# Optimization experiments

Hardware: AMD Instinct MI355X
Metric: run time of the kernel (lower is better)

The kernel has to match this reference:

```python
import jax, jax.numpy as jnp
import numpy as np

B, N, K, H, NC, NL = 512, 128, 16, 16, 6, 4  # batch, atoms, neighbors/atom, h_a, classes, EGNN layers

def _lin(key, fi, fo):
    lim = 1.0 / np.sqrt(fi)
    return jax.random.uniform(key, (fi, fo), jnp.float32, -lim, lim)

def _bias(key, fi, fo):
    lim = 1.0 / np.sqrt(fi)
    return jax.random.uniform(key, (fo,), jnp.float32, -lim, lim)

def setup_inputs():
    key = jax.random.key(0)
    kc, ke, ki, ko, kf, kl = jax.random.split(key, 6)
    coords = jax.random.normal(kc, (B, N, 3), dtype=jnp.float32)
    # fixed adjacency: node i -> (i+1 .. i+K) mod N, same for every frame
    adj = np.zeros((N, N), dtype=np.float32)
    idx = np.arange(N)
    for d in range(1, K + 1):
        adj[idx, (idx + d) % N] = 1.0
    data = jnp.concatenate([coords, jnp.broadcast_to(jnp.asarray(adj), (B, N, N))], axis=-1)  # [B,N,3+N]
    # edge-index construction (host-side; matches torch (edge_inds>0).nonzero().t(), row/col += offset*N)
    off, r, c = np.nonzero(np.broadcast_to(adj > 0.0, (B, N, N)))
    row = jnp.asarray(r + off * N, dtype=jnp.int32)
    col = jnp.asarray(c + off * N, dtype=jnp.int32)
    emb_w = jax.random.normal(ke, (N, H), dtype=jnp.float32)  # atom_emb.weight.data.normal_()
    k1, k2 = jax.random.split(ki); ein_w, ein_b = _lin(k1, H, H), _bias(k2, H, H)
    k1, k2 = jax.random.split(ko); eout_w, eout_b = _lin(k1, H, H), _bias(k2, H, H)
    k1, k2 = jax.random.split(kf); fc_w, fc_b = _lin(k1, H, NC), _bias(k2, H, NC)
    def make_layer(k):
        ks = jax.random.split(k, 11)
        xav = 0.001 * np.sqrt(6.0 / (H + 1))  # coord_mlp last layer: xavier_uniform gain=0.001, no bias
        return dict(
            e1_w=_lin(ks[0], 2 * H + 2, H), e1_b=_bias(ks[1], 2 * H + 2, H),
            e2_w=_lin(ks[2], H, H),        e2_b=_bias(ks[3], H, H),
            n1_w=_lin(ks[4], 2 * H, H),    n1_b=_bias(ks[5], 2 * H, H),
            n2_w=_lin(ks[6], H, H),        n2_b=_bias(ks[7], H, H),
            c1_w=_lin(ks[8], H, H),        c1_b=_bias(ks[9], H, H),
            c2_w=jax.random.uniform(ks[10], (H, 1), jnp.float32, -xav, xav))
    layers = [make_layer(k) for k in jax.random.split(kl, NL)]
    stacked = {name: jnp.stack([l[name] for l in layers]) for name in layers[0]}  # [NL, ...]
    out = dict(data=data, row=row, col=col, emb_w=emb_w, ein_w=ein_w, ein_b=ein_b,
               eout_w=eout_w, eout_b=eout_b, fc_w=fc_w, fc_b=fc_b)
    out.update(stacked)
    return out

def reference(data, row, col, emb_w, ein_w, ein_b, eout_w, eout_b, fc_w, fc_b,
              e1_w, e1_b, e2_w, e2_b, n1_w, n1_b, n2_w, n2_b, c1_w, c1_b, c2_w):
    Bn = data.shape[0] * data.shape[1]  # B*N flattened nodes
    silu = jax.nn.silu
    seg = lambda v: jax.ops.segment_sum(v, row, num_segments=Bn)
    # atom_emb(arange(N)) repeated over batch -> tile embedding table rows
    h = jnp.broadcast_to(emb_w[None, :, :], (data.shape[0], data.shape[1], H)).reshape(Bn, H)
    x = data[:, :, :3].reshape(Bn, 3).astype(jnp.float32)
    e_attr = jnp.ones((row.shape[0], 1), jnp.float32)
    cnt = jnp.maximum(seg(jnp.ones((row.shape[0],), jnp.float32)), 1.0)[:, None]  # for coords_agg='mean'
    h = h @ ein_w + ein_b  # embedding_in
    for l in range(NL):  # E_GCL layers (residual=True, attention=False)
        cd = x[row] - x[col]                                  # [E,3] coord_diff
        radial = jnp.sum(cd * cd, axis=1, keepdims=True)      # [E,1]
        ein = jnp.concatenate([h[row], h[col], radial, e_attr], axis=1)  # [E, 2H+2]
        m = silu(silu(ein @ e1_w[l] + e1_b[l]) @ e2_w[l] + e2_b[l])      # edge_mlp -> [E,H]
        t = silu(m @ c1_w[l] + c1_b[l]) @ c2_w[l]             # coord_mlp -> [E,1]
        x = x + seg(cd * t) / cnt                             # mean-aggregated coord update
        agg_m = seg(m)                                        # scatter-add messages to nodes
        h = h + (silu(jnp.concatenate([h, agg_m], axis=1) @ n1_w[l] + n1_b[l]) @ n2_w[l] + n2_b[l])
    h = h @ eout_w + eout_b  # embedding_out
    prot = jnp.sum(h.reshape(data.shape[0], data.shape[1], H), axis=1) / N  # pooling
    return jax.nn.softmax(prot @ fc_w + fc_b, axis=-1)
```

## Files before the change

### kernel.cpp

```cpp
#include <hip/hip_runtime.h>
#include <math.h>


#define NB   512
#define NN   128
#define HH   16
#define NCLS 6
#define NLAY 4
#define PAD  20

#define W_E1   0
#define W_E1B  544
#define W_E2   560
#define W_E2B  816
#define W_C1   832
#define W_C1B  1088
#define W_C2   1104
#define W_N1   1120
#define W_N1B  1632
#define W_N2   1648
#define W_N2B  1904
#define W_TOT  1920

__device__ __forceinline__ float silu_f(float v) {
    return __fdividef(v, 1.f + __expf(-v));
}

extern "C" __global__ __launch_bounds__(256)
void GraphVampNet_73624329388105_kernel(
    const float* __restrict__ data,
    const float* __restrict__ emb_w,
    const float* __restrict__ ein_w, const float* __restrict__ ein_b,
    const float* __restrict__ eout_w, const float* __restrict__ eout_b,
    const float* __restrict__ fc_w,  const float* __restrict__ fc_b,
    const float* __restrict__ e1_w,  const float* __restrict__ e1_b,
    const float* __restrict__ e2_w,  const float* __restrict__ e2_b,
    const float* __restrict__ n1_w,  const float* __restrict__ n1_b,
    const float* __restrict__ n2_w,  const float* __restrict__ n2_b,
    const float* __restrict__ c1_w,  const float* __restrict__ c1_b,
    const float* __restrict__ c2_w,
    float* __restrict__ out)
{
    __shared__ float h[NN][PAD];
    __shared__ float xs[NN][4];
    __shared__ float pA[NN][PAD];
    __shared__ float pB[NN][PAD];
    __shared__ float part[256][PAD];
    __shared__ __align__(16) float wb[W_TOT];
    __shared__ float hp[HH];
    __shared__ float prot[HH];

    const int b = blockIdx.x;
    const int t = threadIdx.x;

    if (t < NN) {
        const float* dp = data + ((size_t)b * NN + t) * (NN + 3);
        xs[t][0] = dp[0]; xs[t][1] = dp[1]; xs[t][2] = dp[2]; xs[t][3] = 0.f;

        float ev[HH];
        #pragma unroll
        for (int k = 0; k < HH; k++) ev[k] = emb_w[t * HH + k];
        float acc[HH];
        #pragma unroll
        for (int o = 0; o < HH; o++) acc[o] = ein_b[o];
        #pragma unroll
        for (int k = 0; k < HH; k++) {
            const float v = ev[k];
            #pragma unroll
            for (int o = 0; o < HH; o++) acc[o] += v * ein_w[k * HH + o];
        }
        #pragma unroll
        for (int o = 0; o < HH; o++) h[t][o] = acc[o];
    }

    for (int l = 0; l < NLAY; l++) {
        {
            const float* E1W = e1_w + l * 34 * HH;
            wb[W_E1 + t] = E1W[t];
            wb[W_E1 + 256 + t] = E1W[256 + t];
            if (t < 32) wb[W_E1 + 512 + t] = E1W[512 + t];
            wb[W_E2 + t] = e2_w[l * HH * HH + t];
            const float* N1W = n1_w + l * 2 * HH * HH;
            wb[W_N1 + t] = N1W[t];
            wb[W_N1 + 256 + t] = N1W[256 + t];
            wb[W_N2 + t] = n2_w[l * HH * HH + t];
            wb[W_C1 + t] = c1_w[l * HH * HH + t];
            if (t < HH) {
                wb[W_E1B + t] = e1_b[l * HH + t];
                wb[W_E2B + t] = e2_b[l * HH + t];
                wb[W_C1B + t] = c1_b[l * HH + t];
                wb[W_C2  + t] = c2_w[l * HH + t];
                wb[W_N1B + t] = n1_b[l * HH + t];
                wb[W_N2B + t] = n2_b[l * HH + t];
            }
        }
        __syncthreads();

        {
            const int node = t & (NN - 1);
            float hv[HH];
            #pragma unroll
            for (int k = 0; k < HH; k++) hv[k] = h[node][k];
            if (t < NN) {
                float acc[HH];
                #pragma unroll
                for (int o = 0; o < HH; o++) acc[o] = wb[W_E1B + o] + wb[W_E1 + 33 * HH + o];
                #pragma unroll
                for (int k = 0; k < HH; k++) {
                    const float v = hv[k];
                    #pragma unroll
                    for (int o = 0; o < HH; o++) acc[o] += v * wb[W_E1 + k * HH + o];
                }
                #pragma unroll
                for (int o = 0; o < HH; o++) pA[node][o] = acc[o];
            } else {
                float acc[HH];
                #pragma unroll
                for (int o = 0; o < HH; o++) acc[o] = 0.f;
                #pragma unroll
                for (int k = 0; k < HH; k++) {
                    const float v = hv[k];
                    #pragma unroll
                    for (int o = 0; o < HH; o++) acc[o] += v * wb[W_E1 + (16 + k) * HH + o];
                }
                #pragma unroll
                for (int o = 0; o < HH; o++) pB[node][o] = acc[o];
            }
        }
        __syncthreads();

        {
            const int i = t & (NN - 1);
            const int half = t >> 7;
            float pAi[HH];
            #pragma unroll
            for (int o = 0; o < HH; o++) pAi[o] = pA[i][o];
            const float4 xi = *(const float4*)&xs[i][0];
            float aggm[HH];
            #pragma unroll
            for (int o = 0; o < HH; o++) aggm[o] = 0.f;
            float cx0 = 0.f, cx1 = 0.f, cx2 = 0.f;

            #pragma unroll 1
            for (int g = 0; g < 4; g++) {
                unsigned o_col = W_E1 + 32 * HH;
                unsigned o_e2  = W_E2,  o_e2b = W_E2B;
                unsigned o_c1  = W_C1,  o_c1b = W_C1B;
                unsigned o_c2  = W_C2;
                asm volatile("" : "+v"(o_col), "+v"(o_e2), "+v"(o_e2b),
                                  "+v"(o_c1), "+v"(o_c1b), "+v"(o_c2));

                const int dbase = half * 8 + g * 2 + 1;
                const int j0 = (i + dbase) & (NN - 1);
                const int j1 = (i + dbase + 1) & (NN - 1);
                const float4 xj0 = *(const float4*)&xs[j0][0];
                const float4 xj1 = *(const float4*)&xs[j1][0];
                const float a00 = xi.x - xj0.x, a01 = xi.y - xj0.y, a02 = xi.z - xj0.z;
                const float a10 = xi.x - xj1.x, a11 = xi.y - xj1.y, a12 = xi.z - xj1.z;
                const float r0 = a00 * a00 + a01 * a01 + a02 * a02;
                const float r1 = a10 * a10 + a11 * a11 + a12 * a12;

                float m0[HH], m1v[HH];
                #pragma unroll
                for (int q = 0; q < 4; q++) {
                    const float4 wc  = ((const float4*)(wb + o_col))[q];
                    const float4 p0 = *(const float4*)&pB[j0][q * 4];
                    const float4 p1 = *(const float4*)&pB[j1][q * 4];
                    m0[q*4+0]  = silu_f(pAi[q*4+0] + p0.x + r0 * wc.x);
                    m0[q*4+1]  = silu_f(pAi[q*4+1] + p0.y + r0 * wc.y);
                    m0[q*4+2]  = silu_f(pAi[q*4+2] + p0.z + r0 * wc.z);
                    m0[q*4+3]  = silu_f(pAi[q*4+3] + p0.w + r0 * wc.w);
                    m1v[q*4+0] = silu_f(pAi[q*4+0] + p1.x + r1 * wc.x);
                    m1v[q*4+1] = silu_f(pAi[q*4+1] + p1.y + r1 * wc.y);
                    m1v[q*4+2] = silu_f(pAi[q*4+2] + p1.z + r1 * wc.z);
                    m1v[q*4+3] = silu_f(pAi[q*4+3] + p1.w + r1 * wc.w);
                }

                float ac0[HH], ac1[HH];
                #pragma unroll
                for (int q = 0; q < 4; q++) {
                    const float4 bb = ((const float4*)(wb + o_e2b))[q];
                    ac0[q*4+0] = bb.x; ac0[q*4+1] = bb.y; ac0[q*4+2] = bb.z; ac0[q*4+3] = bb.w;
                    ac1[q*4+0] = bb.x; ac1[q*4+1] = bb.y; ac1[q*4+2] = bb.z; ac1[q*4+3] = bb.w;
                }
                #pragma unroll
                for (int k = 0; k < HH; k++) {
                    const float v0 = m0[k], v1 = m1v[k];
                    #pragma unroll
                    for (int q = 0; q < 4; q++) {
                        const float4 w = ((const float4*)(wb + o_e2))[k * 4 + q];
                        ac0[q*4+0] += v0 * w.x; ac0[q*4+1] += v0 * w.y;
                        ac0[q*4+2] += v0 * w.z; ac0[q*4+3] += v0 * w.w;
                        ac1[q*4+0] += v1 * w.x; ac1[q*4+1] += v1 * w.y;
                        ac1[q*4+2] += v1 * w.z; ac1[q*4+3] += v1 * w.w;
                    }
                }
                #pragma unroll
                for (int o = 0; o < HH; o++) {
                    m0[o]  = silu_f(ac0[o]);
                    m1v[o] = silu_f(ac1[o]);
                    aggm[o] += m0[o] + m1v[o];
                }

                #pragma unroll
                for (int q = 0; q < 4; q++) {
                    const float4 bb = ((const float4*)(wb + o_c1b))[q];
                    ac0[q*4+0] = bb.x; ac0[q*4+1] = bb.y; ac0[q*4+2] = bb.z; ac0[q*4+3] = bb.w;
                    ac1[q*4+0] = bb.x; ac1[q*4+1] = bb.y; ac1[q*4+2] = bb.z; ac1[q*4+3] = bb.w;
                }
                #pragma unroll
                for (int k = 0; k < HH; k++) {
                    const float v0 = m0[k], v1 = m1v[k];
                    #pragma unroll
                    for (int q = 0; q < 4; q++) {
                        const float4 w = ((const float4*)(wb + o_c1))[k * 4 + q];
                        ac0[q*4+0] += v0 * w.x; ac0[q*4+1] += v0 * w.y;
                        ac0[q*4+2] += v0 * w.z; ac0[q*4+3] += v0 * w.w;
                        ac1[q*4+0] += v1 * w.x; ac1[q*4+1] += v1 * w.y;
                        ac1[q*4+2] += v1 * w.z; ac1[q*4+3] += v1 * w.w;
                    }
                }
                float t0 = 0.f, t1 = 0.f;
                #pragma unroll
                for (int q = 0; q < 4; q++) {
                    const float4 cw = ((const float4*)(wb + o_c2))[q];
                    t0 += silu_f(ac0[q*4+0]) * cw.x + silu_f(ac0[q*4+1]) * cw.y
                        + silu_f(ac0[q*4+2]) * cw.z + silu_f(ac0[q*4+3]) * cw.w;
                    t1 += silu_f(ac1[q*4+0]) * cw.x + silu_f(ac1[q*4+1]) * cw.y
                        + silu_f(ac1[q*4+2]) * cw.z + silu_f(ac1[q*4+3]) * cw.w;
                }

                cx0 += a00 * t0 + a10 * t1;
                cx1 += a01 * t0 + a11 * t1;
                cx2 += a02 * t0 + a12 * t1;
            }
            #pragma unroll
            for (int o = 0; o < HH; o++) part[t][o] = aggm[o];
            float4 cxv; cxv.x = cx0; cxv.y = cx1; cxv.z = cx2; cxv.w = 0.f;
            *(float4*)&part[t][16] = cxv;
        }
        __syncthreads();

        if (t < NN) {
            float aggm[HH];
            #pragma unroll
            for (int o = 0; o < HH; o++) aggm[o] = part[t][o] + part[t + NN][o];
            float hv[HH];
            #pragma unroll
            for (int k = 0; k < HH; k++) hv[k] = h[t][k];

            float acc[HH];
            #pragma unroll
            for (int o = 0; o < HH; o++) acc[o] = wb[W_N1B + o];
            #pragma unroll
            for (int k = 0; k < HH; k++) {
                const float v = hv[k];
                #pragma unroll
                for (int o = 0; o < HH; o++) acc[o] += v * wb[W_N1 + k * HH + o];
            }
            #pragma unroll
            for (int k = 0; k < HH; k++) {
                const float v = aggm[k];
                #pragma unroll
                for (int o = 0; o < HH; o++) acc[o] += v * wb[W_N1 + (16 + k) * HH + o];
            }
            float u[HH];
            #pragma unroll
            for (int o = 0; o < HH; o++) u[o] = silu_f(acc[o]);

            float acc2[HH];
            #pragma unroll
            for (int o = 0; o < HH; o++) acc2[o] = wb[W_N2B + o];
            #pragma unroll
            for (int k = 0; k < HH; k++) {
                const float v = u[k];
                #pragma unroll
                for (int o = 0; o < HH; o++) acc2[o] += v * wb[W_N2 + k * HH + o];
            }
            #pragma unroll
            for (int o = 0; o < HH; o++) h[t][o] = hv[o] + acc2[o];

            const float inv = 1.f / 16.f;
            xs[t][0] += (part[t][16] + part[t + NN][16]) * inv;
            xs[t][1] += (part[t][17] + part[t + NN][17]) * inv;
            xs[t][2] += (part[t][18] + part[t + NN][18]) * inv;
        }
        __syncthreads();
    }

    if (t < HH) {
        float acc = 0.f;
        for (int i = 0; i < NN; i++) acc += h[i][t];
        hp[t] = acc * (1.f / NN);
    }
    __syncthreads();
    if (t < HH) {
        float acc = eout_b[t];
        #pragma unroll
        for (int k = 0; k < HH; k++) acc += hp[k] * eout_w[k * HH + t];
        prot[t] = acc;
    }
    __syncthreads();
    if (t == 0) {
        float lg[NCLS];
        float mx = -1e30f;
        #pragma unroll
        for (int c = 0; c < NCLS; c++) {
            float acc = fc_b[c];
            #pragma unroll
            for (int k = 0; k < HH; k++) acc += prot[k] * fc_w[k * NCLS + c];
            lg[c] = acc;
            mx = fmaxf(mx, acc);
        }
        float s = 0.f;
        #pragma unroll
        for (int c = 0; c < NCLS; c++) { lg[c] = __expf(lg[c] - mx); s += lg[c]; }
        const float invs = 1.f / s;
        #pragma unroll
        for (int c = 0; c < NCLS; c++) out[b * NCLS + c] = lg[c] * invs;
    }
}

extern "C" void kernel_launch(void* const* d_in, const int* in_sizes, int n_in,
                              void* d_out, int out_size, void* d_ws, size_t ws_size,
                              hipStream_t stream) {
    const float* data   = (const float*)d_in[0];
    const float* emb_w  = (const float*)d_in[3];
    const float* ein_w  = (const float*)d_in[4];
    const float* ein_b  = (const float*)d_in[5];
    const float* eout_w = (const float*)d_in[6];
    const float* eout_b = (const float*)d_in[7];
    const float* fc_w   = (const float*)d_in[8];
    const float* fc_b   = (const float*)d_in[9];
    const float* e1_w   = (const float*)d_in[10];
    const float* e1_b   = (const float*)d_in[11];
    const float* e2_w   = (const float*)d_in[12];
    const float* e2_b   = (const float*)d_in[13];
    const float* n1_w   = (const float*)d_in[14];
    const float* n1_b   = (const float*)d_in[15];
    const float* n2_w   = (const float*)d_in[16];
    const float* n2_b   = (const float*)d_in[17];
    const float* c1_w   = (const float*)d_in[18];
    const float* c1_b   = (const float*)d_in[19];
    const float* c2_w   = (const float*)d_in[20];

    GraphVampNet_73624329388105_kernel<<<NB, 256, 0, stream>>>(
        data, emb_w, ein_w, ein_b, eout_w, eout_b, fc_w, fc_b,
        e1_w, e1_b, e2_w, e2_b, n1_w, n1_b, n2_w, n2_b, c1_w, c1_b, c2_w,
        (float*)d_out);
}
```

Before: 361.9 us.

## Split per-node edge work across four thread groups with 512-thread blocks

Doubles the block size to 512 threads so each node's 16 neighbor edges are handled by four threads (4 edges each) instead of two (8 each), which halves the serial edge loop per thread. The pA and part shared buffers are merged into one union buffer, and the partial message and coordinate sums are reduced three-way into the owner thread. The trade-offs are an extra barrier per layer, threads idling during the node update phases, and tighter register limits from launch_bounds(512,4).

```diff
diff --git a/kernel.cpp b/kernel.cpp
--- a/kernel.cpp
+++ b/kernel.cpp
@@ -3,6 +3,7 @@
 
 
 #define NB   512
+#define NT   512
 #define NN   128
 #define HH   16
 #define NCLS 6
@@ -26,7 +27,7 @@
     return __fdividef(v, 1.f + __expf(-v));
 }
 
-extern "C" __global__ __launch_bounds__(256)
+extern "C" __global__ __launch_bounds__(512, 4)
 void GraphVampNet_73624329388105_kernel(
     const float* __restrict__ data,
     const float* __restrict__ emb_w,
@@ -43,9 +44,8 @@
 {
     __shared__ float h[NN][PAD];
     __shared__ float xs[NN][4];
-    __shared__ float pA[NN][PAD];
     __shared__ float pB[NN][PAD];
-    __shared__ float part[256][PAD];
+    __shared__ __align__(16) float un[384 * PAD];
     __shared__ __align__(16) float wb[W_TOT];
     __shared__ float hp[HH];
     __shared__ float prot[HH];
@@ -72,19 +72,21 @@
         #pragma unroll
         for (int o = 0; o < HH; o++) h[t][o] = acc[o];
     }
+
+    const int i = t & (NN - 1);
+    const int q = t >> 7;
 
     for (int l = 0; l < NLAY; l++) {
         {
             const float* E1W = e1_w + l * 34 * HH;
             wb[W_E1 + t] = E1W[t];
-            wb[W_E1 + 256 + t] = E1W[256 + t];
             if (t < 32) wb[W_E1 + 512 + t] = E1W[512 + t];
-            wb[W_E2 + t] = e2_w[l * HH * HH + t];
-            const float* N1W = n1_w + l * 2 * HH * HH;
-            wb[W_N1 + t] = N1W[t];
-            wb[W_N1 + 256 + t] = N1W[256 + t];
-            wb[W_N2 + t] = n2_w[l * HH * HH + t];
-            wb[W_C1 + t] = c1_w[l * HH * HH + t];
+            wb[W_N1 + t] = n1_w[l * 2 * HH * HH + t];
+            if (t < 256) {
+                wb[W_E2 + t] = e2_w[l * HH * HH + t];
+                wb[W_C1 + t] = c1_w[l * HH * HH + t];
+                wb[W_N2 + t] = n2_w[l * HH * HH + t];
+            }
             if (t < HH) {
                 wb[W_E1B + t] = e1_b[l * HH + t];
                 wb[W_E2B + t] = e2_b[l * HH + t];
@@ -96,7 +98,7 @@
         }
         __syncthreads();
 
-        {
+        if (t < 2 * NN) {
             const int node = t & (NN - 1);
             float hv[HH];
             #pragma unroll
@@ -112,7 +114,7 @@
                     for (int o = 0; o < HH; o++) acc[o] += v * wb[W_E1 + k * HH + o];
                 }
                 #pragma unroll
-                for (int o = 0; o < HH; o++) pA[node][o] = acc[o];
+                for (int o = 0; o < HH; o++) un[node * PAD + o] = acc[o];
             } else {
                 float acc[HH];
                 #pragma unroll
@@ -129,28 +131,24 @@
         }
         __syncthreads();
 
+        float aggm[HH];
+        #pragma unroll
+        for (int o = 0; o < HH; o++) aggm[o] = 0.f;
+        float cx0 = 0.f, cx1 = 0.f, cx2 = 0.f;
         {
-            const int i = t & (NN - 1);
-            const int half = t >> 7;
-            float pAi[HH];
-            #pragma unroll
-            for (int o = 0; o < HH; o++) pAi[o] = pA[i][o];
             const float4 xi = *(const float4*)&xs[i][0];
-            float aggm[HH];
-            #pragma unroll
-            for (int o = 0; o < HH; o++) aggm[o] = 0.f;
-            float cx0 = 0.f, cx1 = 0.f, cx2 = 0.f;
 
             #pragma unroll 1
-            for (int g = 0; g < 4; g++) {
+            for (int g = 0; g < 2; g++) {
                 unsigned o_col = W_E1 + 32 * HH;
                 unsigned o_e2  = W_E2,  o_e2b = W_E2B;
                 unsigned o_c1  = W_C1,  o_c1b = W_C1B;
                 unsigned o_c2  = W_C2;
+                unsigned o_pa  = (unsigned)(i * PAD);
                 asm volatile("" : "+v"(o_col), "+v"(o_e2), "+v"(o_e2b),
-                                  "+v"(o_c1), "+v"(o_c1b), "+v"(o_c2));
-
-                const int dbase = half * 8 + g * 2 + 1;
+                                  "+v"(o_c1), "+v"(o_c1b), "+v"(o_c2), "+v"(o_pa));
+
+                const int dbase = q * 4 + g * 2 + 1;
                 const int j0 = (i + dbase) & (NN - 1);
                 const int j1 = (i + dbase + 1) & (NN - 1);
                 const float4 xj0 = *(const float4*)&xs[j0][0];
@@ -162,37 +160,38 @@
 
                 float m0[HH], m1v[HH];
                 #pragma unroll
-                for (int q = 0; q < 4; q++) {
-                    const float4 wc  = ((const float4*)(wb + o_col))[q];
-                    const float4 p0 = *(const float4*)&pB[j0][q * 4];
-                    const float4 p1 = *(const float4*)&pB[j1][q * 4];
-                    m0[q*4+0]  = silu_f(pAi[q*4+0] + p0.x + r0 * wc.x);
-                    m0[q*4+1]  = silu_f(pAi[q*4+1] + p0.y + r0 * wc.y);
-                    m0[q*4+2]  = silu_f(pAi[q*4+2] + p0.z + r0 * wc.z);
-                    m0[q*4+3]  = silu_f(pAi[q*4+3] + p0.w + r0 * wc.w);
-                    m1v[q*4+0] = silu_f(pAi[q*4+0] + p1.x + r1 * wc.x);
-                    m1v[q*4+1] = silu_f(pAi[q*4+1] + p1.y + r1 * wc.y);
-                    m1v[q*4+2] = silu_f(pAi[q*4+2] + p1.z + r1 * wc.z);
-                    m1v[q*4+3] = silu_f(pAi[q*4+3] + p1.w + r1 * wc.w);
+                for (int qq = 0; qq < 4; qq++) {
+                    const float4 pa = ((const float4*)(un + o_pa))[qq];
+                    const float4 wc = ((const float4*)(wb + o_col))[qq];
+                    const float4 p0 = *(const float4*)&pB[j0][qq * 4];
+                    const float4 p1 = *(const float4*)&pB[j1][qq * 4];
+                    m0[qq*4+0]  = silu_f(pa.x + p0.x + r0 * wc.x);
+                    m0[qq*4+1]  = silu_f(pa.y + p0.y + r0 * wc.y);
+                    m0[qq*4+2]  = silu_f(pa.z + p0.z + r0 * wc.z);
+                    m0[qq*4+3]  = silu_f(pa.w + p0.w + r0 * wc.w);
+                    m1v[qq*4+0] = silu_f(pa.x + p1.x + r1 * wc.x);
+                    m1v[qq*4+1] = silu_f(pa.y + p1.y + r1 * wc.y);
+                    m1v[qq*4+2] = silu_f(pa.z + p1.z + r1 * wc.z);
+                    m1v[qq*4+3] = silu_f(pa.w + p1.w + r1 * wc.w);
                 }
 
                 float ac0[HH], ac1[HH];
                 #pragma unroll
-                for (int q = 0; q < 4; q++) {
-                    const float4 bb = ((const float4*)(wb + o_e2b))[q];
-                    ac0[q*4+0] = bb.x; ac0[q*4+1] = bb.y; ac0[q*4+2] = bb.z; ac0[q*4+3] = bb.w;
-                    ac1[q*4+0] = bb.x; ac1[q*4+1] = bb.y; ac1[q*4+2] = bb.z; ac1[q*4+3] = bb.w;
+                for (int qq = 0; qq < 4; qq++) {
+                    const float4 bb = ((const float4*)(wb + o_e2b))[qq];
+                    ac0[qq*4+0] = bb.x; ac0[qq*4+1] = bb.y; ac0[qq*4+2] = bb.z; ac0[qq*4+3] = bb.w;
+                    ac1[qq*4+0] = bb.x; ac1[qq*4+1] = bb.y; ac1[qq*4+2] = bb.z; ac1[qq*4+3] = bb.w;
                 }
                 #pragma unroll
                 for (int k = 0; k < HH; k++) {
                     const float v0 = m0[k], v1 = m1v[k];
                     #pragma unroll
-                    for (int q = 0; q < 4; q++) {
-                        const float4 w = ((const float4*)(wb + o_e2))[k * 4 + q];
-                        ac0[q*4+0] += v0 * w.x; ac0[q*4+1] += v0 * w.y;
-                        ac0[q*4+2] += v0 * w.z; ac0[q*4+3] += v0 * w.w;
-                        ac1[q*4+0] += v1 * w.x; ac1[q*4+1] += v1 * w.y;
-                        ac1[q*4+2] += v1 * w.z; ac1[q*4+3] += v1 * w.w;
+                    for (int qq = 0; qq < 4; qq++) {
+                        const float4 w = ((const float4*)(wb + o_e2))[k * 4 + qq];
+                        ac0[qq*4+0] += v0 * w.x; ac0[qq*4+1] += v0 * w.y;
+                        ac0[qq*4+2] += v0 * w.z; ac0[qq*4+3] += v0 * w.w;
+                        ac1[qq*4+0] += v1 * w.x; ac1[qq*4+1] += v1 * w.y;
+                        ac1[qq*4+2] += v1 * w.z; ac1[qq*4+3] += v1 * w.w;
                     }
                 }
                 #pragma unroll
@@ -203,48 +202,62 @@
                 }
 
                 #pragma unroll
-                for (int q = 0; q < 4; q++) {
-                    const float4 bb = ((const float4*)(wb + o_c1b))[q];
-                    ac0[q*4+0] = bb.x; ac0[q*4+1] = bb.y; ac0[q*4+2] = bb.z; ac0[q*4+3] = bb.w;
-                    ac1[q*4+0] = bb.x; ac1[q*4+1] = bb.y; ac1[q*4+2] = bb.z; ac1[q*4+3] = bb.w;
+                for (int qq = 0; qq < 4; qq++) {
+                    const float4 bb = ((const float4*)(wb + o_c1b))[qq];
+                    ac0[qq*4+0] = bb.x; ac0[qq*4+1] = bb.y; ac0[qq*4+2] = bb.z; ac0[qq*4+3] = bb.w;
+                    ac1[qq*4+0] = bb.x; ac1[qq*4+1] = bb.y; ac1[qq*4+2] = bb.z; ac1[qq*4+3] = bb.w;
                 }
                 #pragma unroll
                 for (int k = 0; k < HH; k++) {
                     const float v0 = m0[k], v1 = m1v[k];
                     #pragma unroll
-                    for (int q = 0; q < 4; q++) {
-                        const float4 w = ((const float4*)(wb + o_c1))[k * 4 + q];
-                        ac0[q*4+0] += v0 * w.x; ac0[q*4+1] += v0 * w.y;
-                        ac0[q*4+2] += v0 * w.z; ac0[q*4+3] += v0 * w.w;
-                        ac1[q*4+0] += v1 * w.x; ac1[q*4+1] += v1 * w.y;
-                        ac1[q*4+2] += v1 * w.z; ac1[q*4+3] += v1 * w.w;
+                    for (int qq = 0; qq < 4; qq++) {
+                        const float4 w = ((const float4*)(wb + o_c1))[k * 4 + qq];
+                        ac0[qq*4+0] += v0 * w.x; ac0[qq*4+1] += v0 * w.y;
+                        ac0[qq*4+2] += v0 * w.z; ac0[qq*4+3] += v0 * w.w;
+                        ac1[qq*4+0] += v1 * w.x; ac1[qq*4+1] += v1 * w.y;
+                        ac1[qq*4+2] += v1 * w.z; ac1[qq*4+3] += v1 * w.w;
                     }
                 }
                 float t0 = 0.f, t1 = 0.f;
                 #pragma unroll
-                for (int q = 0; q < 4; q++) {
-                    const float4 cw = ((const float4*)(wb + o_c2))[q];
-                    t0 += silu_f(ac0[q*4+0]) * cw.x + silu_f(ac0[q*4+1]) * cw.y
-                        + silu_f(ac0[q*4+2]) * cw.z + silu_f(ac0[q*4+3]) * cw.w;
-                    t1 += silu_f(ac1[q*4+0]) * cw.x + silu_f(ac1[q*4+1]) * cw.y
-                        + silu_f(ac1[q*4+2]) * cw.z + silu_f(ac1[q*4+3]) * cw.w;
+                for (int qq = 0; qq < 4; qq++) {
+                    const float4 cw = ((const float4*)(wb + o_c2))[qq];
+                    t0 += silu_f(ac0[qq*4+0]) * cw.x + silu_f(ac0[qq*4+1]) * cw.y
+                        + silu_f(ac0[qq*4+2]) * cw.z + silu_f(ac0[qq*4+3]) * cw.w;
+                    t1 += silu_f(ac1[qq*4+0]) * cw.x + silu_f(ac1[qq*4+1]) * cw.y
+                        + silu_f(ac1[qq*4+2]) * cw.z + silu_f(ac1[qq*4+3]) * cw.w;
                 }
 
                 cx0 += a00 * t0 + a10 * t1;
                 cx1 += a01 * t0 + a11 * t1;
                 cx2 += a02 * t0 + a12 * t1;
             }
-            #pragma unroll
-            for (int o = 0; o < HH; o++) part[t][o] = aggm[o];
+        }
+        __syncthreads();
+
+        if (t >= NN) {
+            const int r = t - NN;
+            #pragma unroll
+            for (int o = 0; o < HH; o++) un[r * PAD + o] = aggm[o];
             float4 cxv; cxv.x = cx0; cxv.y = cx1; cxv.z = cx2; cxv.w = 0.f;
-            *(float4*)&part[t][16] = cxv;
+            *(float4*)(un + r * PAD + 16) = cxv;
         }
         __syncthreads();
 
         if (t < NN) {
-            float aggm[HH];
-            #pragma unroll
-            for (int o = 0; o < HH; o++) aggm[o] = part[t][o] + part[t + NN][o];
+            float aggt[HH];
+            #pragma unroll
+            for (int o = 0; o < HH; o++)
+                aggt[o] = aggm[o] + un[t * PAD + o] + un[(t + 128) * PAD + o]
+                        + un[(t + 256) * PAD + o];
+            const float sx0 = cx0 + un[t * PAD + 16] + un[(t + 128) * PAD + 16]
+                            + un[(t + 256) * PAD + 16];
+            const float sx1 = cx1 + un[t * PAD + 17] + un[(t + 128) * PAD + 17]
+                            + un[(t + 256) * PAD + 17];
+            const float sx2 = cx2 + un[t * PAD + 18] + un[(t + 128) * PAD + 18]
+                            + un[(t + 256) * PAD + 18];
+
             float hv[HH];
             #pragma unroll
             for (int k = 0; k < HH; k++) hv[k] = h[t][k];
@@ -260,7 +273,7 @@
             }
             #pragma unroll
             for (int k = 0; k < HH; k++) {
-                const float v = aggm[k];
+                const float v = aggt[k];
                 #pragma unroll
                 for (int o = 0; o < HH; o++) acc[o] += v * wb[W_N1 + (16 + k) * HH + o];
             }
@@ -281,16 +294,16 @@
             for (int o = 0; o < HH; o++) h[t][o] = hv[o] + acc2[o];
 
             const float inv = 1.f / 16.f;
-            xs[t][0] += (part[t][16] + part[t + NN][16]) * inv;
-            xs[t][1] += (part[t][17] + part[t + NN][17]) * inv;
-            xs[t][2] += (part[t][18] + part[t + NN][18]) * inv;
+            xs[t][0] += sx0 * inv;
+            xs[t][1] += sx1 * inv;
+            xs[t][2] += sx2 * inv;
         }
         __syncthreads();
     }
 
     if (t < HH) {
         float acc = 0.f;
-        for (int i = 0; i < NN; i++) acc += h[i][t];
+        for (int n = 0; n < NN; n++) acc += h[n][t];
         hp[t] = acc * (1.f / NN);
     }
     __syncthreads();
@@ -344,7 +357,7 @@
     const float* c1_b   = (const float*)d_in[19];
     const float* c2_w   = (const float*)d_in[20];
 
-    GraphVampNet_73624329388105_kernel<<<NB, 256, 0, stream>>>(
+    GraphVampNet_73624329388105_kernel<<<NB, NT, 0, stream>>>(
         data, emb_w, ein_w, ein_b, eout_w, eout_b, fc_w, fc_b,
         e1_w, e1_b, e2_w, e2_b, n1_w, n1_b, n2_w, n2_b, c1_w, c1_b, c2_w,
         (float*)d_out);
```

Result: slower. 385.3 us (+6.5%).
